# Kernel tuning notes

Hardware: AMD Instinct MI355X
Metric: run time of the kernel (lower is better)

The kernel has to match this reference:

```python
import jax, jax.numpy as jnp
import numpy as np
import math

DIM_PER_HEAD = 64

def setup_inputs() -> dict:
    key = jax.random.key(0)
    k1, k2, k3, k4 = jax.random.split(key, 4)
    B, H, S, D = 2, 16, 2048, 64
    mat1 = jax.random.normal(k1, (B, H, S, D), dtype=jnp.float32)
    mat2 = jax.random.normal(k2, (B, H, S, D), dtype=jnp.float32)
    mat3 = jax.random.normal(k3, (B, H, S, D), dtype=jnp.float32)
    bias = jax.random.normal(k4, (1, 1, S, S), dtype=jnp.float32)
    return {"mat1": mat1, "mat2": mat2, "mat3": mat3, "bias": bias}

def reference(mat1, mat2, mat3, bias) -> jnp.ndarray:
    # scale Q, scores = QK^T + bias, softmax over last dim, then @ V
    scale = 1.0 / math.sqrt(DIM_PER_HEAD)
    qk = jnp.einsum('bhqd,bhkd->bhqk', mat1 * scale, mat2)  # [B,H,S,S]
    scores = jax.nn.softmax(qk + bias, axis=-1)
    return jnp.einsum('bhqk,bhkd->bhqd', scores, mat3)
```

## Files before the change

kernel.cpp:

```cpp
#include <hip/hip_runtime.h>
#include <hip/hip_bf16.h>


#define SEQ 2048
#define DH  64
#define BHN 32
#define LOG2E 1.44269504088896f

typedef __attribute__((ext_vector_type(8))) short bf16x8;
typedef __attribute__((ext_vector_type(4))) float f32x4;
typedef __attribute__((ext_vector_type(8))) short short8v;

__device__ inline short f2b(float x) {
    union { float f; unsigned u; } v; v.f = x;
    unsigned r = v.u + 0x7fff + ((v.u >> 16) & 1);
    return (short)(r >> 16);
}

__device__ inline void gl_lds16(const void* g, void* l) {
    __builtin_amdgcn_global_load_lds(
        (const __attribute__((address_space(1))) void*)g,
        (__attribute__((address_space(3))) void*)l, 16, 0, 0);
}

__global__ __launch_bounds__(256)
void prep_kv(const float* __restrict__ K, const float* __restrict__ V,
             short* __restrict__ Kb, short* __restrict__ Vt) {
    __shared__ short t[64 * 72];
    const int tid = threadIdx.x;
    const int bh = blockIdx.x >> 5, st = blockIdx.x & 31, s0 = st * 64;

    {
        const float* Kp = K + ((size_t)bh * SEQ + s0) * DH;
        short* Ko = Kb + ((size_t)bh * SEQ + s0) * DH;
        #pragma unroll
        for (int i = 0; i < 2; ++i) {
            size_t o = (size_t)(tid + i * 256) * 8;
            f32x4 a = *(const f32x4*)(Kp + o);
            f32x4 b = *(const f32x4*)(Kp + o + 4);
            short8v s;
            #pragma unroll
            for (int j = 0; j < 4; ++j) { s[j] = f2b(a[j]); s[4 + j] = f2b(b[j]); }
            *(short8v*)(Ko + o) = s;
        }
    }

    const float* Vb = V + (size_t)bh * SEQ * DH + (size_t)s0 * DH;
    #pragma unroll
    for (int i = 0; i < 4; ++i) {
        int c = tid + i * 256, s = c >> 4, c4 = c & 15;
        f32x4 v = *(const f32x4*)(Vb + s * DH + c4 * 4);
        #pragma unroll
        for (int j = 0; j < 4; ++j) t[s * 72 + c4 * 4 + j] = f2b(v[j]);
    }
    __syncthreads();
    const int d = tid >> 2, part = tid & 3;
    short8v lo, hi;
    #pragma unroll
    for (int j = 0; j < 8; ++j) {
        lo[j] = t[(part * 16 + j) * 72 + d];
        hi[j] = t[(part * 16 + 8 + j) * 72 + d];
    }
    short* outp = Vt + (size_t)bh * DH * SEQ + (size_t)d * SEQ + s0 + part * 16;
    *(short8v*)outp = lo;
    *(short8v*)(outp + 8) = hi;
}

__global__ __launch_bounds__(256, 4)
void mha_main(const float* __restrict__ Q, const float* __restrict__ Bias,
              const short* __restrict__ Kb, const short* __restrict__ Vt,
              float* __restrict__ Out)
{
    __shared__ short lds_k[64 * DH];
    __shared__ short lds_v[DH * 64];
    __shared__ short lds_p[4 * 16 * 64];

    const int tid = threadIdx.x, lane = tid & 63, wave = tid >> 6;
    const int l15 = lane & 15, l4 = lane >> 4;
    const int qb = blockIdx.x & 31, bh = blockIdx.x >> 5;
    const int q0 = qb * 64;

    const float* Qb = Q + (size_t)bh * SEQ * DH;
    const short* Kh = Kb + (size_t)bh * SEQ * DH;
    const short* Vh = Vt + (size_t)bh * DH * SEQ;
    float* Ob = Out + (size_t)bh * SEQ * DH;

    bf16x8 qf[2];
    {
        const float* qp = Qb + (size_t)(q0 + wave * 16 + l15) * DH;
        #pragma unroll
        for (int ks = 0; ks < 2; ++ks) {
            short tmp[8];
            #pragma unroll
            for (int j = 0; j < 8; ++j) tmp[j] = f2b(qp[ks * 32 + l4 * 8 + j] * 0.125f);
            qf[ks] = *reinterpret_cast<bf16x8*>(tmp);
        }
    }

    f32x4 o_acc[4];
    #pragma unroll
    for (int dt = 0; dt < 4; ++dt) o_acc[dt] = f32x4{0.f, 0.f, 0.f, 0.f};
    float l_part[4] = {0.f, 0.f, 0.f, 0.f};

    const short* kg[2]; const short* vg[2]; short* kl[2]; short* vl[2];
    #pragma unroll
    for (int p = 0; p < 2; ++p) {
        int slot = p * 256 + wave * 64 + lane;
        int r_ = slot >> 3;
        int c_ = slot & 7;
        int cg = c_ ^ (r_ & 7);
        kg[p] = Kh + (size_t)r_ * DH + cg * 8;
        vg[p] = Vh + (size_t)r_ * SEQ + cg * 8;
        kl[p] = &lds_k[(size_t)(p * 256 + wave * 64) * 8];
        vl[p] = &lds_v[(size_t)(p * 256 + wave * 64) * 8];
    }
    const float* bp0 = Bias + (size_t)(q0 + wave * 16 + l4 * 4) * SEQ + l15;
    short* pw = &lds_p[wave * 16 * 64];
    const int swz = l15 & 7;

    for (int kt = 0; kt < SEQ / 64; ++kt) {
        const int k0 = kt * 64;
        __syncthreads();
        gl_lds16(kg[0] + (size_t)k0 * DH, kl[0]);
        gl_lds16(kg[1] + (size_t)k0 * DH, kl[1]);
        gl_lds16(vg[0] + k0, vl[0]);
        gl_lds16(vg[1] + k0, vl[1]);

        f32x4 sacc[4];
        const float* bp = bp0 + k0;
        #pragma unroll
        for (int nt = 0; nt < 4; ++nt)
            #pragma unroll
            for (int r = 0; r < 4; ++r)
                sacc[nt][r] = bp[(size_t)r * SEQ + nt * 16];

        __syncthreads();

        #pragma unroll
        for (int ks = 0; ks < 2; ++ks)
            #pragma unroll
            for (int nt = 0; nt < 4; ++nt) {
                int cc = (ks * 4 + l4) ^ swz;
                bf16x8 kf = *(const bf16x8*)&lds_k[(nt * 16 + l15) * DH + cc * 8];
                sacc[nt] = __builtin_amdgcn_mfma_f32_16x16x32_bf16(qf[ks], kf, sacc[nt], 0, 0, 0);
            }

        #pragma unroll
        for (int r = 0; r < 4; ++r) {
            const int prow = l4 * 4 + r;
            const int rsw = prow & 7;
            #pragma unroll
            for (int nt = 0; nt < 4; ++nt) {
                float pv = __builtin_amdgcn_exp2f(sacc[nt][r] * LOG2E);
                l_part[r] += pv;
                int pc = (nt * 2 + (l15 >> 3)) ^ rsw;
                pw[prow * 64 + pc * 8 + (l15 & 7)] = f2b(pv);
            }
        }

        #pragma unroll
        for (int ks = 0; ks < 2; ++ks) {
            int cc = (ks * 4 + l4) ^ swz;
            bf16x8 pf = *(const bf16x8*)&pw[l15 * 64 + cc * 8];
            #pragma unroll
            for (int dt = 0; dt < 4; ++dt) {
                bf16x8 vf = *(const bf16x8*)&lds_v[(dt * 16 + l15) * DH + cc * 8];
                o_acc[dt] = __builtin_amdgcn_mfma_f32_16x16x32_bf16(pf, vf, o_acc[dt], 0, 0, 0);
            }
        }
    }

    #pragma unroll
    for (int r = 0; r < 4; ++r) {
        float s = l_part[r];
        #pragma unroll
        for (int m = 1; m < 16; m <<= 1) s += __shfl_xor(s, m, 64);
        l_part[r] = s;
    }

    #pragma unroll
    for (int r = 0; r < 4; ++r) {
        float inv = 1.0f / l_part[r];
        float* op = Ob + (size_t)(q0 + wave * 16 + l4 * 4 + r) * DH + l15;
        #pragma unroll
        for (int dt = 0; dt < 4; ++dt) op[dt * 16] = o_acc[dt][r] * inv;
    }
}

extern "C" void kernel_launch(void* const* d_in, const int* in_sizes, int n_in,
                              void* d_out, int out_size, void* d_ws, size_t ws_size,
                              hipStream_t stream) {
    const float* Q    = (const float*)d_in[0];
    const float* K    = (const float*)d_in[1];
    const float* V    = (const float*)d_in[2];
    const float* Bias = (const float*)d_in[3];
    float* O          = (float*)d_out;

    short* Kb = (short*)d_ws;
    short* Vt = Kb + (size_t)BHN * SEQ * DH;

    prep_kv<<<dim3(BHN * 32), dim3(256), 0, stream>>>(K, V, Kb, Vt);
    mha_main<<<dim3(BHN * 32), dim3(256), 0, stream>>>(Q, Bias, Kb, Vt, O);
}
```

Baseline: 168.6 us.

## Process two 64-key tiles per barrier pair to halve synchronization

Widens the key-loop step from 64 to 128 by loading two K/V sub-tiles into doubled LDS buffers per iteration and preloading bias for both halves. This halves the number of __syncthreads pairs and puts more outstanding global loads in flight per stage. In exchange it raises LDS use (about 40KB per block), which may limit occupancy under launch_bounds(256,4), and it raises register pressure from the extra bias values.

```diff
diff --git a/kernel.cpp b/kernel.cpp
--- a/kernel.cpp
+++ b/kernel.cpp
@@ -5,6 +5,7 @@
 #define SEQ 2048
 #define DH  64
 #define BHN 32
+#define NTILE (SEQ / 128)
 #define LOG2E 1.44269504088896f
 
 typedef __attribute__((ext_vector_type(8))) short bf16x8;
@@ -71,8 +72,8 @@
               const short* __restrict__ Kb, const short* __restrict__ Vt,
               float* __restrict__ Out)
 {
-    __shared__ short lds_k[64 * DH];
-    __shared__ short lds_v[DH * 64];
+    __shared__ short lds_k[2][64 * DH];
+    __shared__ short lds_v[2][64 * DH];
     __shared__ short lds_p[4 * 16 * 64];
 
     const int tid = threadIdx.x, lane = tid & 63, wave = tid >> 6;
@@ -111,61 +112,89 @@
         int cg = c_ ^ (r_ & 7);
         kg[p] = Kh + (size_t)r_ * DH + cg * 8;
         vg[p] = Vh + (size_t)r_ * SEQ + cg * 8;
-        kl[p] = &lds_k[(size_t)(p * 256 + wave * 64) * 8];
-        vl[p] = &lds_v[(size_t)(p * 256 + wave * 64) * 8];
+        kl[p] = &lds_k[0][(size_t)slot * 8];
+        vl[p] = &lds_v[0][(size_t)slot * 8];
     }
     const float* bp0 = Bias + (size_t)(q0 + wave * 16 + l4 * 4) * SEQ + l15;
     short* pw = &lds_p[wave * 16 * 64];
     const int swz = l15 & 7;
 
-    for (int kt = 0; kt < SEQ / 64; ++kt) {
-        const int k0 = kt * 64;
+    for (int kt = 0; kt < NTILE; ++kt) {
+        const int k0 = kt * 128;
         __syncthreads();
-        gl_lds16(kg[0] + (size_t)k0 * DH, kl[0]);
-        gl_lds16(kg[1] + (size_t)k0 * DH, kl[1]);
-        gl_lds16(vg[0] + k0, vl[0]);
-        gl_lds16(vg[1] + k0, vl[1]);
+
+        #pragma unroll
+        for (int hh = 0; hh < 2; ++hh) {
+            const size_t koff = (size_t)(k0 + hh * 64) * DH;
+            const int voff = k0 + hh * 64;
+            const int lo = hh * (64 * DH);
+            gl_lds16(kg[0] + koff, kl[0] + lo);
+            gl_lds16(kg[1] + koff, kl[1] + lo);
+            gl_lds16(vg[0] + voff, vl[0] + lo);
+            gl_lds16(vg[1] + voff, vl[1] + lo);
+        }
 
         f32x4 sacc[4];
-        const float* bp = bp0 + k0;
-        #pragma unroll
-        for (int nt = 0; nt < 4; ++nt)
-            #pragma unroll
-            for (int r = 0; r < 4; ++r)
-                sacc[nt][r] = bp[(size_t)r * SEQ + nt * 16];
+        float b1[4][4];
+        {
+            const float* bp = bp0 + k0;
+            #pragma unroll
+            for (int nt = 0; nt < 4; ++nt)
+                #pragma unroll
+                for (int r = 0; r < 4; ++r) {
+                    sacc[nt][r]  = bp[(size_t)r * SEQ + nt * 16];
+                    b1[nt][r]    = bp[(size_t)r * SEQ + nt * 16 + 64];
+                }
+        }
 
         __syncthreads();
 
         #pragma unroll
-        for (int ks = 0; ks < 2; ++ks)
-            #pragma unroll
-            for (int nt = 0; nt < 4; ++nt) {
+        for (int hh = 0; hh < 2; ++hh) {
+            if (hh) {
+                #pragma unroll
+                for (int nt = 0; nt < 4; ++nt)
+                    #pragma unroll
+                    for (int r = 0; r < 4; ++r)
+                        sacc[nt][r] = b1[nt][r];
+            }
+
+            const short* lk = lds_k[hh];
+            const short* lv = lds_v[hh];
+
+            #pragma unroll
+            for (int ks = 0; ks < 2; ++ks)
+                #pragma unroll
+                for (int nt = 0; nt < 4; ++nt) {
+                    int cc = (ks * 4 + l4) ^ swz;
+                    bf16x8 kf = *(const bf16x8*)&lk[(nt * 16 + l15) * DH + cc * 8];
+                    sacc[nt] = __builtin_amdgcn_mfma_f32_16x16x32_bf16(
+                        qf[ks], kf, sacc[nt], 0, 0, 0);
+                }
+
+            #pragma unroll
+            for (int r = 0; r < 4; ++r) {
+                const int prow = l4 * 4 + r;
+                const int rsw = prow & 7;
+                #pragma unroll
+                for (int nt = 0; nt < 4; ++nt) {
+                    float pv = __builtin_amdgcn_exp2f(sacc[nt][r] * LOG2E);
+                    l_part[r] += pv;
+                    int pc = (nt * 2 + (l15 >> 3)) ^ rsw;
+                    pw[prow * 64 + pc * 8 + (l15 & 7)] = f2b(pv);
+                }
+            }
+
+            #pragma unroll
+            for (int ks = 0; ks < 2; ++ks) {
                 int cc = (ks * 4 + l4) ^ swz;
-                bf16x8 kf = *(const bf16x8*)&lds_k[(nt * 16 + l15) * DH + cc * 8];
-                sacc[nt] = __builtin_amdgcn_mfma_f32_16x16x32_bf16(qf[ks], kf, sacc[nt], 0, 0, 0);
-            }
-
-        #pragma unroll
-        for (int r = 0; r < 4; ++r) {
-            const int prow = l4 * 4 + r;
-            const int rsw = prow & 7;
-            #pragma unroll
-            for (int nt = 0; nt < 4; ++nt) {
-                float pv = __builtin_amdgcn_exp2f(sacc[nt][r] * LOG2E);
-                l_part[r] += pv;
-                int pc = (nt * 2 + (l15 >> 3)) ^ rsw;
-                pw[prow * 64 + pc * 8 + (l15 & 7)] = f2b(pv);
-            }
-        }
-
-        #pragma unroll
-        for (int ks = 0; ks < 2; ++ks) {
-            int cc = (ks * 4 + l4) ^ swz;
-            bf16x8 pf = *(const bf16x8*)&pw[l15 * 64 + cc * 8];
-            #pragma unroll
-            for (int dt = 0; dt < 4; ++dt) {
-                bf16x8 vf = *(const bf16x8*)&lds_v[(dt * 16 + l15) * DH + cc * 8];
-                o_acc[dt] = __builtin_amdgcn_mfma_f32_16x16x32_bf16(pf, vf, o_acc[dt], 0, 0, 0);
+                bf16x8 pf = *(const bf16x8*)&pw[l15 * 64 + cc * 8];
+                #pragma unroll
+                for (int dt = 0; dt < 4; ++dt) {
+                    bf16x8 vf = *(const bf16x8*)&lv[(dt * 16 + l15) * DH + cc * 8];
+                    o_acc[dt] = __builtin_amdgcn_mfma_f32_16x16x32_bf16(
+                        pf, vf, o_acc[dt], 0, 0, 0);
+                }
             }
         }
     }
```

After: 169.1 us. About the same (+0.3%).

## Split attention key range across two blocks and combine partial outputs

Applied to the files above, without the earlier changes.

Each query tile is now processed by two blocks that each cover half of the key tiles. They write unnormalized partial outputs and row sums, and a new combine kernel adds them and normalizes. The aim is to double the grid size so the GPU's compute units stay busier, with the launch-bounds occupancy hint raised from 4 to 6. The cost is an extra kernel launch and an extra round trip of a full fp32 output buffer through memory. The split path runs only when the workspace is large enough, and the old path is kept as a fallback.

```diff
diff --git a/kernel.cpp b/kernel.cpp
--- a/kernel.cpp
+++ b/kernel.cpp
@@ -5,6 +5,7 @@
 #define SEQ 2048
 #define DH  64
 #define BHN 32
+#define NTILE (SEQ / 64)
 #define LOG2E 1.44269504088896f
 
 typedef __attribute__((ext_vector_type(8))) short bf16x8;
@@ -66,10 +67,12 @@
     *(short8v*)(outp + 8) = hi;
 }
 
-__global__ __launch_bounds__(256, 4)
+template<int SPLIT>
+__global__ __launch_bounds__(256, 6)
 void mha_main(const float* __restrict__ Q, const float* __restrict__ Bias,
               const short* __restrict__ Kb, const short* __restrict__ Vt,
-              float* __restrict__ Out)
+              float* __restrict__ Out, float* __restrict__ Opart,
+              float* __restrict__ Lp0, float* __restrict__ Lp1)
 {
     __shared__ short lds_k[64 * DH];
     __shared__ short lds_v[DH * 64];
@@ -77,17 +80,20 @@
 
     const int tid = threadIdx.x, lane = tid & 63, wave = tid >> 6;
     const int l15 = lane & 15, l4 = lane >> 4;
-    const int qb = blockIdx.x & 31, bh = blockIdx.x >> 5;
+    const int bid = blockIdx.x;
+    const int half = SPLIT ? (bid >> 10) : 0;
+    const int rest = SPLIT ? (bid & 1023) : bid;
+    const int qb = rest & 31, bh = rest >> 5;
     const int q0 = qb * 64;
+    const int qw = q0 + wave * 16;
 
     const float* Qb = Q + (size_t)bh * SEQ * DH;
     const short* Kh = Kb + (size_t)bh * SEQ * DH;
     const short* Vh = Vt + (size_t)bh * DH * SEQ;
-    float* Ob = Out + (size_t)bh * SEQ * DH;
 
     bf16x8 qf[2];
     {
-        const float* qp = Qb + (size_t)(q0 + wave * 16 + l15) * DH;
+        const float* qp = Qb + (size_t)(qw + l15) * DH;
         #pragma unroll
         for (int ks = 0; ks < 2; ++ks) {
             short tmp[8];
@@ -114,11 +120,14 @@
         kl[p] = &lds_k[(size_t)(p * 256 + wave * 64) * 8];
         vl[p] = &lds_v[(size_t)(p * 256 + wave * 64) * 8];
     }
-    const float* bp0 = Bias + (size_t)(q0 + wave * 16 + l4 * 4) * SEQ + l15;
+    const float* bp0 = Bias + (size_t)(qw + l4 * 4) * SEQ + l15;
     short* pw = &lds_p[wave * 16 * 64];
     const int swz = l15 & 7;
 
-    for (int kt = 0; kt < SEQ / 64; ++kt) {
+    const int kt0 = SPLIT ? half * (NTILE / 2) : 0;
+    const int kt1 = SPLIT ? kt0 + (NTILE / 2) : NTILE;
+
+    for (int kt = kt0; kt < kt1; ++kt) {
         const int k0 = kt * 64;
         __syncthreads();
         gl_lds16(kg[0] + (size_t)k0 * DH, kl[0]);
@@ -178,13 +187,50 @@
         l_part[r] = s;
     }
 
-    #pragma unroll
-    for (int r = 0; r < 4; ++r) {
-        float inv = 1.0f / l_part[r];
-        float* op = Ob + (size_t)(q0 + wave * 16 + l4 * 4 + r) * DH + l15;
-        #pragma unroll
-        for (int dt = 0; dt < 4; ++dt) op[dt * 16] = o_acc[dt][r] * inv;
-    }
+    if (!SPLIT) {
+        float* Ob = Out + (size_t)bh * SEQ * DH;
+        #pragma unroll
+        for (int r = 0; r < 4; ++r) {
+            float inv = 1.0f / l_part[r];
+            float* op = Ob + (size_t)(qw + l4 * 4 + r) * DH + l15;
+            #pragma unroll
+            for (int dt = 0; dt < 4; ++dt) op[dt * 16] = o_acc[dt][r] * inv;
+        }
+    } else {
+        float* ob = (half ? Opart : Out) + (size_t)bh * SEQ * DH;
+        #pragma unroll
+        for (int r = 0; r < 4; ++r) {
+            float* op = ob + (size_t)(qw + l4 * 4 + r) * DH + l15;
+            #pragma unroll
+            for (int dt = 0; dt < 4; ++dt) op[dt * 16] = o_acc[dt][r];
+        }
+        float* Lh = (half ? Lp1 : Lp0) + (size_t)bh * SEQ;
+        if (l15 == 0) {
+            #pragma unroll
+            for (int r = 0; r < 4; ++r) Lh[qw + l4 * 4 + r] = l_part[r];
+        }
+    }
+}
+
+__global__ __launch_bounds__(256)
+void combine(float* __restrict__ Out, const float* __restrict__ Opart,
+             const float* __restrict__ L0v, const float* __restrict__ L1v)
+{
+    const int gid = blockIdx.x * 256 + threadIdx.x;
+    const int row = gid >> 3;
+    const int d0 = (gid & 7) * 8;
+    const float li = 1.0f / (L0v[row] + L1v[row]);
+    float* op = Out + (size_t)row * DH + d0;
+    const float* pp = Opart + (size_t)row * DH + d0;
+    f32x4 a0 = *(const f32x4*)op,       a1 = *(const f32x4*)pp;
+    f32x4 b0 = *(const f32x4*)(op + 4), b1 = *(const f32x4*)(pp + 4);
+    #pragma unroll
+    for (int j = 0; j < 4; ++j) {
+        a0[j] = (a0[j] + a1[j]) * li;
+        b0[j] = (b0[j] + b1[j]) * li;
+    }
+    *(f32x4*)op = a0;
+    *(f32x4*)(op + 4) = b0;
 }
 
 extern "C" void kernel_launch(void* const* d_in, const int* in_sizes, int n_in,
@@ -198,7 +244,23 @@
 
     short* Kb = (short*)d_ws;
     short* Vt = Kb + (size_t)BHN * SEQ * DH;
+    float* Opart = (float*)(Vt + (size_t)BHN * SEQ * DH);
+    float* L0v = Opart + (size_t)BHN * SEQ * DH;
+    float* L1v = L0v + (size_t)BHN * SEQ;
+
+    const size_t need_split =
+        (size_t)2 * BHN * SEQ * DH * sizeof(short) +
+        ((size_t)BHN * SEQ * DH + 2 * (size_t)BHN * SEQ) * sizeof(float);
 
     prep_kv<<<dim3(BHN * 32), dim3(256), 0, stream>>>(K, V, Kb, Vt);
-    mha_main<<<dim3(BHN * 32), dim3(256), 0, stream>>>(Q, Bias, Kb, Vt, O);
-}
+
+    if (ws_size >= need_split) {
+        mha_main<1><<<dim3(2 * BHN * 32), dim3(256), 0, stream>>>(
+            Q, Bias, Kb, Vt, O, Opart, L0v, L1v);
+        combine<<<dim3(BHN * SEQ * DH / (256 * 8)), dim3(256), 0, stream>>>(
+            O, Opart, L0v, L1v);
+    } else {
+        mha_main<0><<<dim3(BHN * 32), dim3(256), 0, stream>>>(
+            Q, Bias, Kb, Vt, O, Opart, L0v, L1v);
+    }
+}
```

After: 211.6 us. 1.26x slower.
